# Kernel optimization log

Hardware: AMD Instinct MI355X
Metric: run time of the kernel (lower is better)

The kernel has to match this reference:

```python
import jax, jax.numpy as jnp
import numpy as np

B, S, D, H, HD = 8, 1, 4096, 32, 128
MAX_SEQ, AL, FF = 2048, 10, 11008
START_POS = 2047
EPS = 1e-5


def setup_inputs() -> dict:
    key = jax.random.key(0)
    ks = jax.random.split(key, 12)
    # real RoPE angles for the single decode position START_POS
    inv_freq = 1.0 / (10000.0 ** (np.arange(0, HD, 2, dtype=np.float32) / HD))  # [HD/2]
    ang = (np.float32(START_POS) * inv_freq)[None, :]  # [S=1, HD/2]
    return {
        "x": jax.random.normal(ks[0], (B, S, D), jnp.float32),
        "adapter": jax.random.normal(ks[1], (1, AL, D), jnp.float32),
        "cache_k": jax.random.normal(ks[2], (B, MAX_SEQ, H, HD), jnp.float32),
        "cache_v": jax.random.normal(ks[3], (B, MAX_SEQ, H, HD), jnp.float32),
        "freqs_cos": jnp.cos(jnp.asarray(ang)),
        "freqs_sin": jnp.sin(jnp.asarray(ang)),
        "wq": jax.random.normal(ks[4], (D, D), jnp.float32) * 0.02,
        "wk": jax.random.normal(ks[5], (D, D), jnp.float32) * 0.02,
        "wv": jax.random.normal(ks[6], (D, D), jnp.float32) * 0.02,
        "wo": jax.random.normal(ks[7], (D, D), jnp.float32) * 0.02,
        "gate": jax.random.normal(ks[8], (1, H, 1, 1), jnp.float32) * 0.5,
        "attn_norm_w": jnp.ones((D,), jnp.float32),
        "ffn_norm_w": jnp.ones((D,), jnp.float32),
        "w1": jax.random.normal(ks[9], (D, FF), jnp.float32) * 0.02,
        "w2": jax.random.normal(ks[10], (FF, D), jnp.float32) * 0.02,
        "w3": jax.random.normal(ks[11], (D, FF), jnp.float32) * 0.02,
        "start_pos": START_POS,
    }


def _rmsnorm(x, w, eps=EPS):
    xf = x.astype(jnp.float32)
    return (xf * jax.lax.rsqrt(jnp.mean(xf * xf, axis=-1, keepdims=True) + eps)).astype(x.dtype) * w


def _rope(t, cos, sin):
    # t: [B,S,H,HD]; pairs are interleaved as in view_as_complex(reshape(..,-1,2))
    tr = t.reshape(*t.shape[:-1], HD // 2, 2)
    a, b = tr[..., 0], tr[..., 1]
    c = cos[None, :, None, :]
    s = sin[None, :, None, :]
    out = jnp.stack([a * c - b * s, a * s + b * c], axis=-1)
    return out.reshape(t.shape)


def _sdpa(q, k, v):
    # q:[B,H,S,HD], k/v:[B,H,K,HD]
    scores = jnp.einsum("bhqd,bhkd->bhqk", q, k) / jnp.sqrt(jnp.float32(HD))
    p = jax.nn.softmax(scores.astype(jnp.float32), axis=-1).astype(q.dtype)
    return jnp.einsum("bhqk,bhkd->bhqd", p, v)


def reference(x, adapter, cache_k, cache_v, freqs_cos, freqs_sin,
              wq, wk, wv, wo, gate, attn_norm_w, ffn_norm_w, w1, w2, w3, start_pos):
    bsz, seqlen, _ = x.shape
    # --- attention sub-block ---
    xn = _rmsnorm(x, attn_norm_w)
    xq = (xn @ wq).reshape(bsz, seqlen, H, HD)
    xk = (xn @ wk).reshape(bsz, seqlen, H, HD)
    xv = (xn @ wv).reshape(bsz, seqlen, H, HD)
    xq = _rope(xq, freqs_cos, freqs_sin)
    xk = _rope(xk, freqs_cos, freqs_sin)
    # KV-cache append
    cache_k = jax.lax.dynamic_update_slice(cache_k, xk, (0, start_pos, 0, 0))
    cache_v = jax.lax.dynamic_update_slice(cache_v, xv, (0, start_pos, 0, 0))
    keys = cache_k[:, : start_pos + seqlen].transpose(0, 2, 1, 3)   # [B,H,K,HD]
    values = cache_v[:, : start_pos + seqlen].transpose(0, 2, 1, 3)
    q = xq.transpose(0, 2, 1, 3)                                     # [B,H,S,HD]
    out = _sdpa(q, keys, values)                                     # [B,H,S,HD]
    # adapter-gated cross attention (adapter keys/values: no RoPE, shared over batch)
    ak = (adapter @ wk).reshape(AL, H, HD).transpose(1, 0, 2)        # [H,AL,HD]
    av = (adapter @ wv).reshape(AL, H, HD).transpose(1, 0, 2)        # [H,AL,HD]
    a_scores = jnp.einsum("bhqd,hkd->bhqk", q, ak) / jnp.sqrt(jnp.float32(HD))
    a_p = jax.nn.softmax(a_scores.astype(jnp.float32), axis=-1).astype(q.dtype)
    a_out = jnp.einsum("bhqk,hkd->bhqd", a_p, av)
    out = out + jnp.tanh(gate) * a_out
    attn_out = out.transpose(0, 2, 1, 3).reshape(bsz, seqlen, H * HD) @ wo
    h = x + attn_out
    # --- feed-forward sub-block (SwiGLU) ---
    hn = _rmsnorm(h, ffn_norm_w)
    ffn = (jax.nn.silu(hn @ w1) * (hn @ w3)) @ w2
    return h + ffn
```

## Files before the change

kernel.cpp:

```cpp
#include <hip/hip_runtime.h>
#include <cmath>

#define D_ 4096
#define H_ 32
#define HD_ 128
#define B_ 8
#define MAXSEQ_ 2048
#define AL_ 10
#define FF_ 11008
#define SCALE_ 0.08838834764831845f
#define EPS_ 1e-5f

__global__ __launch_bounds__(256) void norm_adapter_k(const float* __restrict__ x,
                                                      const float* __restrict__ w,
                                                      const float* __restrict__ adapter,
                                                      float* __restrict__ xa) {
  int b = blockIdx.x, tid = threadIdx.x;
  if (b < 8) {
    const float* xr = x + (size_t)b * D_;
    float ss = 0.f;
    for (int i = tid; i < D_; i += 256) { float v = xr[i]; ss += v * v; }
    __shared__ float red[256];
    red[tid] = ss; __syncthreads();
    for (int s = 128; s; s >>= 1) { if (tid < s) red[tid] += red[tid + s]; __syncthreads(); }
    float r = rsqrtf(red[0] / (float)D_ + EPS_);
    float* o = xa + (size_t)b * D_;
    for (int i = tid; i < D_; i += 256) o[i] = xr[i] * r * w[i];
  } else {
    int r = b - 8;
    const float4* src = (const float4*)(adapter + (size_t)r * D_);
    float4* dst = (float4*)(xa + (size_t)(8 + r) * D_);
    for (int i = tid; i < D_ / 4; i += 256) dst[i] = src[i];
  }
}

__global__ __launch_bounds__(256) void rmsnorm_k(const float* __restrict__ in,
                                                 const float* __restrict__ w,
                                                 float* __restrict__ out) {
  int b = blockIdx.x, tid = threadIdx.x;
  const float* x = in + (size_t)b * D_;
  float ss = 0.f;
  for (int i = tid; i < D_; i += 256) { float v = x[i]; ss += v * v; }
  __shared__ float red[256];
  red[tid] = ss; __syncthreads();
  for (int s = 128; s; s >>= 1) { if (tid < s) red[tid] += red[tid + s]; __syncthreads(); }
  float r = rsqrtf(red[0] / (float)D_ + EPS_);
  float* o = out + (size_t)b * D_;
  for (int i = tid; i < D_; i += 256) o[i] = x[i] * r * w[i];
}

template<int NR, int ROWS, int CHUNK, int UNROLL>
__device__ __forceinline__ void gemv_core(
    const float4* __restrict__ W4, const float (*xs)[ROWS],
    int i0, int N4, int j4, int r0, float* __restrict__ P, size_t pb, int N) {
  float4 acc[NR];
#pragma unroll
  for (int r = 0; r < NR; ++r) acc[r] = make_float4(0.f, 0.f, 0.f, 0.f);
  for (int iu = 0; iu < CHUNK; iu += UNROLL) {
    float4 w[UNROLL];
#pragma unroll
    for (int u = 0; u < UNROLL; ++u)
      w[u] = W4[(size_t)(i0 + iu + u) * N4 + j4];
#pragma unroll
    for (int u = 0; u < UNROLL; ++u) {
#pragma unroll
      for (int r = 0; r < NR; ++r) {
        float xv = xs[iu + u][r0 + r];
        acc[r].x += xv * w[u].x; acc[r].y += xv * w[u].y;
        acc[r].z += xv * w[u].z; acc[r].w += xv * w[u].w;
      }
    }
  }
#pragma unroll
  for (int r = 0; r < NR; ++r)
    *(float4*)&P[(pb + r) * (size_t)N + (size_t)4 * j4] = acc[r];
}

template<int ROWS, int RPG, int CHUNK, int UNROLL>
__global__ __launch_bounds__(256, 1) void gemv_rs(
    const float* __restrict__ X,
    const float* __restrict__ Wa, const float* __restrict__ Wb, const float* __restrict__ Wc,
    float* __restrict__ P, int N, int K) {
  const float* W = (blockIdx.z == 0) ? Wa : (blockIdx.z == 1) ? Wb : Wc;
  __shared__ float xs[CHUNK][ROWS];
  int tid = threadIdx.x;
  int i0 = blockIdx.y * CHUNK;
  for (int idx = tid; idx < ROWS * CHUNK; idx += 256) {
    int r = idx / CHUNK, ii = idx - r * CHUNK;
    xs[ii][r] = X[(size_t)r * K + i0 + ii];
  }
  __syncthreads();
  int wave = tid >> 6, lane = tid & 63;
  int r0 = wave * RPG;
  int N4 = N >> 2;
  int j4 = blockIdx.x * 64 + lane;
  const float4* W4 = (const float4*)W;
  size_t pb = ((size_t)blockIdx.z * gridDim.y + blockIdx.y) * ROWS + r0;
  constexpr int LAST = ROWS - 3 * RPG;
  if (r0 + RPG <= ROWS)
    gemv_core<RPG, ROWS, CHUNK, UNROLL>(W4, xs, i0, N4, j4, r0, P, pb, N);
  else if (LAST > 0)
    gemv_core<(LAST > 0 ? LAST : 1), ROWS, CHUNK, UNROLL>(W4, xs, i0, N4, j4, r0, P, pb, N);
}

__global__ __launch_bounds__(256) void reduce3_rope_k(
    const float* __restrict__ P, const float* __restrict__ fc, const float* __restrict__ fs,
    float* __restrict__ Ya, float* __restrict__ Yb, float* __restrict__ Yc) {
  int z = blockIdx.z;
  int i4 = blockIdx.x * 256 + threadIdx.x;
  const float4* P4 = (const float4*)P;
  size_t base = (size_t)z * 16 * 18432 + i4;
  float4 s = make_float4(0.f, 0.f, 0.f, 0.f);
#pragma unroll
  for (int c = 0; c < 16; ++c) {
    float4 v = P4[base + (size_t)c * 18432];
    s.x += v.x; s.y += v.y; s.z += v.z; s.w += v.w;
  }
  int row = i4 >> 10;
  if (z < 2 && row < 8) {
    int c0 = (i4 & 1023) << 2;
    int p0 = (c0 & 127) >> 1;
    float ca = fc[p0], sa = fs[p0], cb = fc[p0 + 1], sb = fs[p0 + 1];
    float4 r;
    r.x = s.x * ca - s.y * sa; r.y = s.x * sa + s.y * ca;
    r.z = s.z * cb - s.w * sb; r.w = s.z * sb + s.w * cb;
    s = r;
  }
  float4* Y = (float4*)(z == 0 ? Ya : z == 1 ? Yb : Yc);
  Y[i4] = s;
}

__global__ __launch_bounds__(256) void reduceB_k(const float* __restrict__ P,
                                                 const float* __restrict__ base,
                                                 float* __restrict__ Y, int n4, int nc) {
  int i4 = blockIdx.x * 256 + threadIdx.x;
  if (i4 >= n4) return;
  const float4* P4 = (const float4*)P;
  float4 s = ((const float4*)base)[i4];
  for (int c = 0; c < nc; ++c) {
    float4 v = P4[(size_t)c * n4 + i4];
    s.x += v.x; s.y += v.y; s.z += v.z; s.w += v.w;
  }
  ((float4*)Y)[i4] = s;
}

__global__ __launch_bounds__(256) void reduce_silu_k(const float* __restrict__ P,
                                                     float* __restrict__ gb) {
  int i4 = blockIdx.x * 256 + threadIdx.x;
  const float4* P4 = (const float4*)P;
  float4 a = make_float4(0.f, 0.f, 0.f, 0.f);
  float4 b = make_float4(0.f, 0.f, 0.f, 0.f);
#pragma unroll
  for (int c = 0; c < 8; ++c) {
    float4 u = P4[(size_t)c * 22016 + i4];
    float4 v = P4[(size_t)(8 + c) * 22016 + i4];
    a.x += u.x; a.y += u.y; a.z += u.z; a.w += u.w;
    b.x += v.x; b.y += v.y; b.z += v.z; b.w += v.w;
  }
  float4 o;
  o.x = (a.x / (1.f + __expf(-a.x))) * b.x;
  o.y = (a.y / (1.f + __expf(-a.y))) * b.y;
  o.z = (a.z / (1.f + __expf(-a.z))) * b.z;
  o.w = (a.w / (1.f + __expf(-a.w))) * b.w;
  ((float4*)gb)[i4] = o;
}

__global__ __launch_bounds__(256) void attn_partial(
    const float* __restrict__ qp,
    const float* __restrict__ ck,
    const float* __restrict__ cv,
    float* __restrict__ part) {
  int idx = blockIdx.x;
  int c = idx & 7, bh = idx >> 3;
  int h = bh & 31, b = bh >> 5;
  int tid = threadIdx.x, wave = tid >> 6, lane = tid & 63;
  int half = lane >> 5, l32 = lane & 31;
  int t0 = c * 256 + wave * 64;
  const float4 qv = *(const float4*)&qp[(size_t)b * D_ + h * HD_ + 4 * l32];
  const size_t kvbase = ((size_t)b * MAXSEQ_) * (H_ * HD_) + (size_t)h * HD_ + 4 * l32;
  float m = -INFINITY, l = 0.f;
  float4 o = make_float4(0.f, 0.f, 0.f, 0.f);
#pragma unroll 4
  for (int i = 0; i < 32; ++i) {
    int t = t0 + 2 * i + half;
    size_t off = kvbase + (size_t)t * (H_ * HD_);
    float4 kv = *(const float4*)&ck[off];
    float s = qv.x * kv.x + qv.y * kv.y + qv.z * kv.z + qv.w * kv.w;
    s += __shfl_xor(s, 16); s += __shfl_xor(s, 8);
    s += __shfl_xor(s, 4);  s += __shfl_xor(s, 2); s += __shfl_xor(s, 1);
    s *= SCALE_;
    if (t == MAXSEQ_ - 1) s = -1e30f;
    float mn = fmaxf(m, s);
    float r = __expf(m - mn), p = __expf(s - mn);
    float4 vv = *(const float4*)&cv[off];
    o.x = o.x * r + p * vv.x; o.y = o.y * r + p * vv.y;
    o.z = o.z * r + p * vv.z; o.w = o.w * r + p * vv.w;
    l = l * r + p; m = mn;
  }
  float mo = __shfl_xor(m, 32);
  float M = fmaxf(m, mo);
  float e = __expf(m - M);
  o.x *= e; o.y *= e; o.z *= e; o.w *= e; l *= e;
  o.x += __shfl_xor(o.x, 32); o.y += __shfl_xor(o.y, 32);
  o.z += __shfl_xor(o.z, 32); o.w += __shfl_xor(o.w, 32);
  l += __shfl_xor(l, 32);
  float* po = &part[((size_t)idx * 4 + wave) * 132];
  if (lane == 0) { po[0] = M; po[1] = l; }
  if (half == 0) *(float4*)&po[4 + 4 * l32] = o;
}

__global__ __launch_bounds__(128) void attn_combine(
    const float* __restrict__ part,
    const float* __restrict__ qp,
    const float* __restrict__ kvk,
    const float* __restrict__ kvv,
    const float* __restrict__ gate,
    float* __restrict__ attn) {
  int bh = blockIdx.x;
  int h = bh & 31, b = bh >> 5;
  int tid = threadIdx.x;
  const float* pb = &part[(size_t)bh * 32 * 132];
  __shared__ float sm[32], sl[32];
  if (tid < 32) { sm[tid] = pb[tid * 132]; sl[tid] = pb[tid * 132 + 1]; }
  __syncthreads();
  float M = -INFINITY;
  for (int c = 0; c < 32; ++c) M = fmaxf(M, sm[c]);
  float L = 0.f, O = 0.f;
  for (int c = 0; c < 32; ++c) {
    float e = __expf(sm[c] - M);
    L += e * sl[c];
    O += e * pb[c * 132 + 4 + tid];
  }
  size_t qi = (size_t)b * D_ + h * HD_ + tid;
  float qd = qp[qi];
  __shared__ float red[128];
  __shared__ float sa[10];
  red[tid] = qd * kvk[qi]; __syncthreads();
  for (int s = 64; s; s >>= 1) { if (tid < s) red[tid] += red[tid + s]; __syncthreads(); }
  float s_new = red[0] * SCALE_;
  __syncthreads();
  float M2 = fmaxf(M, s_new);
  float eM = __expf(M - M2), eN = __expf(s_new - M2);
  L = L * eM + eN;
  O = O * eM + eN * kvv[qi];
  float main_out = O / L;
  for (int j = 0; j < 10; ++j) {
    float prod = qd * kvk[(size_t)(8 + j) * D_ + h * HD_ + tid];
    red[tid] = prod; __syncthreads();
    for (int s = 64; s; s >>= 1) { if (tid < s) red[tid] += red[tid + s]; __syncthreads(); }
    if (tid == 0) sa[j] = red[0] * SCALE_;
    __syncthreads();
  }
  float ma = -INFINITY;
  for (int j = 0; j < 10; ++j) ma = fmaxf(ma, sa[j]);
  float la = 0.f, pj[10];
  for (int j = 0; j < 10; ++j) { pj[j] = __expf(sa[j] - ma); la += pj[j]; }
  float ao = 0.f;
  for (int j = 0; j < 10; ++j) ao += pj[j] * kvv[(size_t)(8 + j) * D_ + h * HD_ + tid];
  ao /= la;
  float g = tanhf(gate[h]);
  attn[qi] = main_out + g * ao;
}

extern "C" void kernel_launch(void* const* d_in, const int* in_sizes, int n_in,
                              void* d_out, int out_size, void* d_ws, size_t ws_size,
                              hipStream_t stream) {
  (void)in_sizes; (void)n_in; (void)out_size; (void)ws_size;
  const float* x       = (const float*)d_in[0];
  const float* adapter = (const float*)d_in[1];
  const float* ck      = (const float*)d_in[2];
  const float* cv      = (const float*)d_in[3];
  const float* fc      = (const float*)d_in[4];
  const float* fs      = (const float*)d_in[5];
  const float* wq      = (const float*)d_in[6];
  const float* wk      = (const float*)d_in[7];
  const float* wv      = (const float*)d_in[8];
  const float* wo      = (const float*)d_in[9];
  const float* gate    = (const float*)d_in[10];
  const float* anw     = (const float*)d_in[11];
  const float* fnw     = (const float*)d_in[12];
  const float* w1      = (const float*)d_in[13];
  const float* w2      = (const float*)d_in[14];
  const float* w3      = (const float*)d_in[15];
  float* out = (float*)d_out;

  float* ws      = (float*)d_ws;
  float* xa      = ws;
  float* qp      = xa + 18 * D_;
  float* kp      = qp + 18 * D_;
  float* vp      = kp + 18 * D_;
  float* attn    = vp + 18 * D_;
  float* hbuf    = attn + 8 * D_;
  float* hn      = hbuf + 8 * D_;
  float* gb      = hn + 8 * D_;
  float* scratch = gb + 8 * FF_;

  norm_adapter_k<<<18, 256, 0, stream>>>(x, anw, adapter, xa);
  gemv_rs<18, 5, 256, 16><<<dim3(16, 16, 3), 256, 0, stream>>>(xa, wq, wk, wv, scratch, D_, D_);
  reduce3_rope_k<<<dim3(72, 1, 3), 256, 0, stream>>>(scratch, fc, fs, qp, kp, vp);
  attn_partial<<<2048, 256, 0, stream>>>(qp, ck, cv, scratch);
  attn_combine<<<256, 128, 0, stream>>>(scratch, qp, kp, vp, gate, attn);
  gemv_rs<8, 2, 128, 16><<<dim3(16, 32, 1), 256, 0, stream>>>(attn, wo, wo, wo, scratch, D_, D_);
  reduceB_k<<<32, 256, 0, stream>>>(scratch, x, hbuf, 8192, 32);
  rmsnorm_k<<<8, 256, 0, stream>>>(hbuf, fnw, hn);
  gemv_rs<8, 2, 512, 16><<<dim3(43, 8, 2), 256, 0, stream>>>(hn, w1, w3, w3, scratch, FF_, D_);
  reduce_silu_k<<<86, 256, 0, stream>>>(scratch, gb);
  gemv_rs<8, 2, 344, 8><<<dim3(16, 32, 1), 256, 0, stream>>>(gb, w2, w2, w2, scratch, D_, FF_);
  reduceB_k<<<32, 256, 0, stream>>>(scratch, hbuf, out, 8192, 32);
}
```

Before: 398.3 us.

## Restructure decode attention so each block streams full KV rows across all heads

Measured after the change: 412.6 us. 1.04x slower.

```diff
diff --git a/kernel.cpp b/kernel.cpp
--- a/kernel.cpp
+++ b/kernel.cpp
@@ -8,6 +8,7 @@
 #define MAXSEQ_ 2048
 #define AL_ 10
 #define FF_ 11008
+#define NC_ 128
 #define SCALE_ 0.08838834764831845f
 #define EPS_ 1e-5f
 
@@ -130,10 +131,10 @@
   Y[i4] = s;
 }
 
-__global__ __launch_bounds__(256) void reduceB_k(const float* __restrict__ P,
+__global__ __launch_bounds__(128) void reduceB_k(const float* __restrict__ P,
                                                  const float* __restrict__ base,
                                                  float* __restrict__ Y, int n4, int nc) {
-  int i4 = blockIdx.x * 256 + threadIdx.x;
+  int i4 = blockIdx.x * 128 + threadIdx.x;
   if (i4 >= n4) return;
   const float4* P4 = (const float4*)P;
   float4 s = ((const float4*)base)[i4];
@@ -144,9 +145,9 @@
   ((float4*)Y)[i4] = s;
 }
 
-__global__ __launch_bounds__(256) void reduce_silu_k(const float* __restrict__ P,
+__global__ __launch_bounds__(128) void reduce_silu_k(const float* __restrict__ P,
                                                      float* __restrict__ gb) {
-  int i4 = blockIdx.x * 256 + threadIdx.x;
+  int i4 = blockIdx.x * 128 + threadIdx.x;
   const float4* P4 = (const float4*)P;
   float4 a = make_float4(0.f, 0.f, 0.f, 0.f);
   float4 b = make_float4(0.f, 0.f, 0.f, 0.f);
@@ -165,48 +166,48 @@
   ((float4*)gb)[i4] = o;
 }
 
-__global__ __launch_bounds__(256) void attn_partial(
+__global__ __launch_bounds__(256, 4) void attn_partial(
     const float* __restrict__ qp,
     const float* __restrict__ ck,
     const float* __restrict__ cv,
     float* __restrict__ part) {
-  int idx = blockIdx.x;
-  int c = idx & 7, bh = idx >> 3;
-  int h = bh & 31, b = bh >> 5;
+  int c = blockIdx.x, b = blockIdx.y;
   int tid = threadIdx.x, wave = tid >> 6, lane = tid & 63;
-  int half = lane >> 5, l32 = lane & 31;
-  int t0 = c * 256 + wave * 64;
-  const float4 qv = *(const float4*)&qp[(size_t)b * D_ + h * HD_ + 4 * l32];
-  const size_t kvbase = ((size_t)b * MAXSEQ_) * (H_ * HD_) + (size_t)h * HD_ + 4 * l32;
+  int hl = lane >> 3;
+  int h = wave * 8 + hl;
+  int d0 = (lane & 7) << 4;
+  const float4* q4 = (const float4*)&qp[(size_t)b * D_ + h * HD_ + d0];
+  float4 q0 = q4[0], q1 = q4[1], q2 = q4[2], q3 = q4[3];
+  int t0 = c * 16;
+  size_t base = ((size_t)(b * MAXSEQ_ + t0)) * D_ + (size_t)h * HD_ + d0;
   float m = -INFINITY, l = 0.f;
-  float4 o = make_float4(0.f, 0.f, 0.f, 0.f);
+  float4 o0 = make_float4(0.f,0.f,0.f,0.f), o1 = o0, o2 = o0, o3 = o0;
 #pragma unroll 4
-  for (int i = 0; i < 32; ++i) {
-    int t = t0 + 2 * i + half;
-    size_t off = kvbase + (size_t)t * (H_ * HD_);
-    float4 kv = *(const float4*)&ck[off];
-    float s = qv.x * kv.x + qv.y * kv.y + qv.z * kv.z + qv.w * kv.w;
-    s += __shfl_xor(s, 16); s += __shfl_xor(s, 8);
-    s += __shfl_xor(s, 4);  s += __shfl_xor(s, 2); s += __shfl_xor(s, 1);
+  for (int i = 0; i < 16; ++i) {
+    size_t off = base + (size_t)i * D_;
+    const float4* kp4 = (const float4*)&ck[off];
+    float4 k0 = kp4[0], k1 = kp4[1], k2 = kp4[2], k3 = kp4[3];
+    float s = q0.x*k0.x + q0.y*k0.y + q0.z*k0.z + q0.w*k0.w
+            + q1.x*k1.x + q1.y*k1.y + q1.z*k1.z + q1.w*k1.w
+            + q2.x*k2.x + q2.y*k2.y + q2.z*k2.z + q2.w*k2.w
+            + q3.x*k3.x + q3.y*k3.y + q3.z*k3.z + q3.w*k3.w;
+    s += __shfl_xor(s, 1); s += __shfl_xor(s, 2); s += __shfl_xor(s, 4);
     s *= SCALE_;
-    if (t == MAXSEQ_ - 1) s = -1e30f;
+    if (t0 + i == MAXSEQ_ - 1) s = -1e30f;
     float mn = fmaxf(m, s);
     float r = __expf(m - mn), p = __expf(s - mn);
-    float4 vv = *(const float4*)&cv[off];
-    o.x = o.x * r + p * vv.x; o.y = o.y * r + p * vv.y;
-    o.z = o.z * r + p * vv.z; o.w = o.w * r + p * vv.w;
+    const float4* vp4 = (const float4*)&cv[off];
+    float4 v0 = vp4[0], v1 = vp4[1], v2 = vp4[2], v3 = vp4[3];
+    o0.x = o0.x*r + p*v0.x; o0.y = o0.y*r + p*v0.y; o0.z = o0.z*r + p*v0.z; o0.w = o0.w*r + p*v0.w;
+    o1.x = o1.x*r + p*v1.x; o1.y = o1.y*r + p*v1.y; o1.z = o1.z*r + p*v1.z; o1.w = o1.w*r + p*v1.w;
+    o2.x = o2.x*r + p*v2.x; o2.y = o2.y*r + p*v2.y; o2.z = o2.z*r + p*v2.z; o2.w = o2.w*r + p*v2.w;
+    o3.x = o3.x*r + p*v3.x; o3.y = o3.y*r + p*v3.y; o3.z = o3.z*r + p*v3.z; o3.w = o3.w*r + p*v3.w;
     l = l * r + p; m = mn;
   }
-  float mo = __shfl_xor(m, 32);
-  float M = fmaxf(m, mo);
-  float e = __expf(m - M);
-  o.x *= e; o.y *= e; o.z *= e; o.w *= e; l *= e;
-  o.x += __shfl_xor(o.x, 32); o.y += __shfl_xor(o.y, 32);
-  o.z += __shfl_xor(o.z, 32); o.w += __shfl_xor(o.w, 32);
-  l += __shfl_xor(l, 32);
-  float* po = &part[((size_t)idx * 4 + wave) * 132];
-  if (lane == 0) { po[0] = M; po[1] = l; }
-  if (half == 0) *(float4*)&po[4 + 4 * l32] = o;
+  float* po = &part[(((size_t)b * NC_ + c) * H_ + h) * 132];
+  if ((lane & 7) == 0) { po[0] = m; po[1] = l; }
+  float4* po4 = (float4*)&po[4 + d0];
+  po4[0] = o0; po4[1] = o1; po4[2] = o2; po4[3] = o3;
 }
 
 __global__ __launch_bounds__(128) void attn_combine(
@@ -219,40 +220,47 @@
   int bh = blockIdx.x;
   int h = bh & 31, b = bh >> 5;
   int tid = threadIdx.x;
-  const float* pb = &part[(size_t)bh * 32 * 132];
-  __shared__ float sm[32], sl[32];
-  if (tid < 32) { sm[tid] = pb[tid * 132]; sl[tid] = pb[tid * 132 + 1]; }
+  int wave = tid >> 6, lane = tid & 63;
+  const size_t cs = (size_t)H_ * 132;
+  const float* pb = &part[((size_t)b * NC_ * H_ + h) * 132];
+  __shared__ float sm[NC_], sl[NC_], red[NC_];
+  sm[tid] = pb[cs * tid];
+  sl[tid] = pb[cs * tid + 1];
   __syncthreads();
-  float M = -INFINITY;
-  for (int c = 0; c < 32; ++c) M = fmaxf(M, sm[c]);
+  red[tid] = sm[tid]; __syncthreads();
+  for (int s = 64; s; s >>= 1) { if (tid < s) red[tid] = fmaxf(red[tid], red[tid + s]); __syncthreads(); }
+  float M = red[0];
   float L = 0.f, O = 0.f;
-  for (int c = 0; c < 32; ++c) {
-    float e = __expf(sm[c] - M);
-    L += e * sl[c];
-    O += e * pb[c * 132 + 4 + tid];
+#pragma unroll 4
+  for (int c2 = 0; c2 < NC_; ++c2) {
+    float e = __expf(sm[c2] - M);
+    L += e * sl[c2];
+    O += e * pb[cs * c2 + 4 + tid];
   }
   size_t qi = (size_t)b * D_ + h * HD_ + tid;
   float qd = qp[qi];
-  __shared__ float red[128];
-  __shared__ float sa[10];
-  red[tid] = qd * kvk[qi]; __syncthreads();
-  for (int s = 64; s; s >>= 1) { if (tid < s) red[tid] += red[tid + s]; __syncthreads(); }
-  float s_new = red[0] * SCALE_;
+  __shared__ float s2[2][12];
+  {
+    float pr = qd * kvk[qi];
+    pr += __shfl_xor(pr, 32); pr += __shfl_xor(pr, 16); pr += __shfl_xor(pr, 8);
+    pr += __shfl_xor(pr, 4);  pr += __shfl_xor(pr, 2);  pr += __shfl_xor(pr, 1);
+    if (lane == 0) s2[wave][10] = pr;
+  }
+  for (int j = 0; j < 10; ++j) {
+    float pr = qd * kvk[(size_t)(8 + j) * D_ + h * HD_ + tid];
+    pr += __shfl_xor(pr, 32); pr += __shfl_xor(pr, 16); pr += __shfl_xor(pr, 8);
+    pr += __shfl_xor(pr, 4);  pr += __shfl_xor(pr, 2);  pr += __shfl_xor(pr, 1);
+    if (lane == 0) s2[wave][j] = pr;
+  }
   __syncthreads();
+  float s_new = (s2[0][10] + s2[1][10]) * SCALE_;
   float M2 = fmaxf(M, s_new);
   float eM = __expf(M - M2), eN = __expf(s_new - M2);
   L = L * eM + eN;
   O = O * eM + eN * kvv[qi];
   float main_out = O / L;
-  for (int j = 0; j < 10; ++j) {
-    float prod = qd * kvk[(size_t)(8 + j) * D_ + h * HD_ + tid];
-    red[tid] = prod; __syncthreads();
-    for (int s = 64; s; s >>= 1) { if (tid < s) red[tid] += red[tid + s]; __syncthreads(); }
-    if (tid == 0) sa[j] = red[0] * SCALE_;
-    __syncthreads();
-  }
-  float ma = -INFINITY;
-  for (int j = 0; j < 10; ++j) ma = fmaxf(ma, sa[j]);
+  float ma = -INFINITY, sa[10];
+  for (int j = 0; j < 10; ++j) { sa[j] = (s2[0][j] + s2[1][j]) * SCALE_; ma = fmaxf(ma, sa[j]); }
   float la = 0.f, pj[10];
   for (int j = 0; j < 10; ++j) { pj[j] = __expf(sa[j] - ma); la += pj[j]; }
   float ao = 0.f;
@@ -298,13 +306,13 @@
   norm_adapter_k<<<18, 256, 0, stream>>>(x, anw, adapter, xa);
   gemv_rs<18, 5, 256, 16><<<dim3(16, 16, 3), 256, 0, stream>>>(xa, wq, wk, wv, scratch, D_, D_);
   reduce3_rope_k<<<dim3(72, 1, 3), 256, 0, stream>>>(scratch, fc, fs, qp, kp, vp);
-  attn_partial<<<2048, 256, 0, stream>>>(qp, ck, cv, scratch);
+  attn_partial<<<dim3(NC_, 8), 256, 0, stream>>>(qp, ck, cv, scratch);
   attn_combine<<<256, 128, 0, stream>>>(scratch, qp, kp, vp, gate, attn);
   gemv_rs<8, 2, 128, 16><<<dim3(16, 32, 1), 256, 0, stream>>>(attn, wo, wo, wo, scratch, D_, D_);
-  reduceB_k<<<32, 256, 0, stream>>>(scratch, x, hbuf, 8192, 32);
+  reduceB_k<<<64, 128, 0, stream>>>(scratch, x, hbuf, 8192, 32);
   rmsnorm_k<<<8, 256, 0, stream>>>(hbuf, fnw, hn);
   gemv_rs<8, 2, 512, 16><<<dim3(43, 8, 2), 256, 0, stream>>>(hn, w1, w3, w3, scratch, FF_, D_);
-  reduce_silu_k<<<86, 256, 0, stream>>>(scratch, gb);
+  reduce_silu_k<<<172, 128, 0, stream>>>(scratch, gb);
   gemv_rs<8, 2, 344, 8><<<dim3(16, 32, 1), 256, 0, stream>>>(gb, w2, w2, w2, scratch, D_, FF_);
-  reduceB_k<<<32, 256, 0, stream>>>(scratch, hbuf, out, 8192, 32);
-}
+  reduceB_k<<<64, 128, 0, stream>>>(scratch, hbuf, out, 8192, 32);
+}
```

## Fuse decoder layer into one persistent cooperative kernel with grid syncs

Applied to the files above, without the earlier changes.

Result: slower. 777.7 us (+95.3%).

```diff
diff --git a/kernel.cpp b/kernel.cpp
--- a/kernel.cpp
+++ b/kernel.cpp
@@ -1,5 +1,8 @@
 #include <hip/hip_runtime.h>
+#include <hip/hip_cooperative_groups.h>
 #include <cmath>
+
+namespace cg = cooperative_groups;
 
 #define D_ 4096
 #define H_ 32
@@ -8,8 +11,305 @@
 #define MAXSEQ_ 2048
 #define AL_ 10
 #define FF_ 11008
+#define NBLK 256
 #define SCALE_ 0.08838834764831845f
 #define EPS_ 1e-5f
+
+template<int NR, int ROWS, int CHUNK, int UNROLL>
+__device__ __forceinline__ void gemv_core(
+    const float4* __restrict__ W4, const float (*xs)[ROWS],
+    int i0, int N4, int j4, int r0, float* __restrict__ P, size_t pb, int N) {
+  float4 acc[NR];
+#pragma unroll
+  for (int r = 0; r < NR; ++r) acc[r] = make_float4(0.f, 0.f, 0.f, 0.f);
+  for (int iu = 0; iu < CHUNK; iu += UNROLL) {
+    float4 w[UNROLL];
+#pragma unroll
+    for (int u = 0; u < UNROLL; ++u)
+      w[u] = W4[(size_t)(i0 + iu + u) * N4 + j4];
+#pragma unroll
+    for (int u = 0; u < UNROLL; ++u) {
+#pragma unroll
+      for (int r = 0; r < NR; ++r) {
+        float xv = xs[iu + u][r0 + r];
+        acc[r].x += xv * w[u].x; acc[r].y += xv * w[u].y;
+        acc[r].z += xv * w[u].z; acc[r].w += xv * w[u].w;
+      }
+    }
+  }
+#pragma unroll
+  for (int r = 0; r < NR; ++r)
+    *(float4*)&P[(pb + r) * (size_t)N + (size_t)4 * j4] = acc[r];
+}
+
+template<int ROWS, int RPG, int CHUNK, int UNROLL>
+__device__ __forceinline__ void gemv_phase(
+    const float* __restrict__ X, const float* __restrict__ W, float* __restrict__ P,
+    int N, int K, int bx, int by, int zoff, float* smem, int tid) {
+  int i0 = by * CHUNK;
+  for (int idx = tid; idx < ROWS * CHUNK; idx += 256) {
+    int r = idx / CHUNK, ii = idx - r * CHUNK;
+    smem[ii * ROWS + r] = X[(size_t)r * K + i0 + ii];
+  }
+  __syncthreads();
+  int wave = tid >> 6, lane = tid & 63;
+  int r0 = wave * RPG;
+  int N4 = N >> 2;
+  int j4 = bx * 64 + lane;
+  size_t pb = (size_t)zoff * ROWS + r0;
+  const float (*xs)[ROWS] = (const float (*)[ROWS])smem;
+  constexpr int LAST = ROWS - 3 * RPG;
+  if (r0 + RPG <= ROWS)
+    gemv_core<RPG, ROWS, CHUNK, UNROLL>((const float4*)W, xs, i0, N4, j4, r0, P, pb, N);
+  else if (LAST > 0)
+    gemv_core<(LAST > 0 ? LAST : 1), ROWS, CHUNK, UNROLL>((const float4*)W, xs, i0, N4, j4, r0, P, pb, N);
+  __syncthreads();
+}
+
+__device__ __forceinline__ void rmsnorm_phase(const float* __restrict__ in,
+                                              const float* __restrict__ w,
+                                              float* __restrict__ outp,
+                                              int b, float* red, int tid) {
+  const float* xr = in + (size_t)b * D_;
+  float ss = 0.f;
+  for (int i = tid; i < D_; i += 256) { float v = xr[i]; ss += v * v; }
+  red[tid] = ss; __syncthreads();
+  for (int s = 128; s; s >>= 1) { if (tid < s) red[tid] += red[tid + s]; __syncthreads(); }
+  float r = rsqrtf(red[0] / (float)D_ + EPS_);
+  __syncthreads();
+  float* o = outp + (size_t)b * D_;
+  for (int i = tid; i < D_; i += 256) o[i] = xr[i] * r * w[i];
+}
+
+__global__ __launch_bounds__(256, 1) void mega_k(
+    const float* __restrict__ x, const float* __restrict__ adapter,
+    const float* __restrict__ ck, const float* __restrict__ cv,
+    const float* __restrict__ fc, const float* __restrict__ fs,
+    const float* __restrict__ wq, const float* __restrict__ wk,
+    const float* __restrict__ wv, const float* __restrict__ wo,
+    const float* __restrict__ gate, const float* __restrict__ anw,
+    const float* __restrict__ fnw, const float* __restrict__ w1,
+    const float* __restrict__ w2, const float* __restrict__ w3,
+    float* __restrict__ out, float* __restrict__ ws) {
+  cg::grid_group grid = cg::this_grid();
+  __shared__ float smem[4608];
+  int blk = blockIdx.x, tid = threadIdx.x;
+
+  float* xa      = ws;
+  float* qp      = xa + 18 * D_;
+  float* kp      = qp + 18 * D_;
+  float* vp      = kp + 18 * D_;
+  float* attn    = vp + 18 * D_;
+  float* hbuf    = attn + 8 * D_;
+  float* hn      = hbuf + 8 * D_;
+  float* gb      = hn + 8 * D_;
+  float* scratch = gb + 8 * FF_;
+
+  if (blk < 8) {
+    rmsnorm_phase(x, anw, xa, blk, smem, tid);
+  } else if (blk < 18) {
+    int r = blk - 8;
+    const float4* src = (const float4*)(adapter + (size_t)r * D_);
+    float4* dst = (float4*)(xa + (size_t)(8 + r) * D_);
+    for (int i = tid; i < D_ / 4; i += 256) dst[i] = src[i];
+  }
+  grid.sync();
+
+  for (int vb = blk; vb < 768; vb += NBLK) {
+    int bx = vb & 15, by = (vb >> 4) & 15, z = vb >> 8;
+    const float* W = (z == 0) ? wq : (z == 1) ? wk : wv;
+    gemv_phase<18, 5, 256, 16>(xa, W, scratch, D_, D_, bx, by, z * 16 + by, smem, tid);
+  }
+  grid.sync();
+
+  for (int vb = blk; vb < 216; vb += NBLK) {
+    int z = vb / 72, xb = vb - z * 72;
+    int i4 = xb * 256 + tid;
+    const float4* P4 = (const float4*)scratch;
+    size_t base = (size_t)z * 16 * 18432 + i4;
+    float4 s = make_float4(0.f, 0.f, 0.f, 0.f);
+#pragma unroll
+    for (int c = 0; c < 16; ++c) {
+      float4 v = P4[base + (size_t)c * 18432];
+      s.x += v.x; s.y += v.y; s.z += v.z; s.w += v.w;
+    }
+    int row = i4 >> 10;
+    if (z < 2 && row < 8) {
+      int c0 = (i4 & 1023) << 2;
+      int p0 = (c0 & 127) >> 1;
+      float ca = fc[p0], sa = fs[p0], cb = fc[p0 + 1], sb = fs[p0 + 1];
+      float4 r;
+      r.x = s.x * ca - s.y * sa; r.y = s.x * sa + s.y * ca;
+      r.z = s.z * cb - s.w * sb; r.w = s.z * sb + s.w * cb;
+      s = r;
+    }
+    float4* Y = (float4*)(z == 0 ? qp : z == 1 ? kp : vp);
+    Y[i4] = s;
+  }
+  grid.sync();
+
+  {
+    int b = blk >> 5, c = blk & 31;
+    int wave = tid >> 6, lane = tid & 63;
+    int hl = lane >> 3, h = wave * 8 + hl;
+    int d0 = (lane & 7) << 4;
+    const float4* q4 = (const float4*)&qp[(size_t)b * D_ + h * HD_ + d0];
+    float4 q0 = q4[0], q1 = q4[1], q2 = q4[2], q3 = q4[3];
+    int t0 = c * 64;
+    size_t base = ((size_t)(b * MAXSEQ_ + t0)) * D_ + (size_t)h * HD_ + d0;
+    float m = -INFINITY, l = 0.f;
+    float4 o0 = make_float4(0.f,0.f,0.f,0.f), o1 = o0, o2 = o0, o3 = o0;
+#pragma unroll 4
+    for (int i = 0; i < 64; ++i) {
+      size_t off = base + (size_t)i * D_;
+      const float4* kp4 = (const float4*)&ck[off];
+      float4 k0 = kp4[0], k1 = kp4[1], k2 = kp4[2], k3 = kp4[3];
+      float s = q0.x*k0.x + q0.y*k0.y + q0.z*k0.z + q0.w*k0.w
+              + q1.x*k1.x + q1.y*k1.y + q1.z*k1.z + q1.w*k1.w
+              + q2.x*k2.x + q2.y*k2.y + q2.z*k2.z + q2.w*k2.w
+              + q3.x*k3.x + q3.y*k3.y + q3.z*k3.z + q3.w*k3.w;
+      s += __shfl_xor(s, 1); s += __shfl_xor(s, 2); s += __shfl_xor(s, 4);
+      s *= SCALE_;
+      if (t0 + i == MAXSEQ_ - 1) s = -1e30f;
+      float mn = fmaxf(m, s);
+      float r = __expf(m - mn), p = __expf(s - mn);
+      const float4* vp4 = (const float4*)&cv[off];
+      float4 v0 = vp4[0], v1 = vp4[1], v2 = vp4[2], v3 = vp4[3];
+      o0.x = o0.x*r + p*v0.x; o0.y = o0.y*r + p*v0.y; o0.z = o0.z*r + p*v0.z; o0.w = o0.w*r + p*v0.w;
+      o1.x = o1.x*r + p*v1.x; o1.y = o1.y*r + p*v1.y; o1.z = o1.z*r + p*v1.z; o1.w = o1.w*r + p*v1.w;
+      o2.x = o2.x*r + p*v2.x; o2.y = o2.y*r + p*v2.y; o2.z = o2.z*r + p*v2.z; o2.w = o2.w*r + p*v2.w;
+      o3.x = o3.x*r + p*v3.x; o3.y = o3.y*r + p*v3.y; o3.z = o3.z*r + p*v3.z; o3.w = o3.w*r + p*v3.w;
+      l = l * r + p; m = mn;
+    }
+    float* po = &scratch[(((size_t)b * 32 + c) * H_ + h) * 132];
+    if ((lane & 7) == 0) { po[0] = m; po[1] = l; }
+    float4* po4 = (float4*)&po[4 + d0];
+    po4[0] = o0; po4[1] = o1; po4[2] = o2; po4[3] = o3;
+  }
+  grid.sync();
+
+  for (int vb = blk; vb < 128; vb += NBLK) {
+    int half = tid >> 7, t2 = tid & 127;
+    int bh = vb * 2 + half;
+    int h = bh & 31, b = bh >> 5;
+    int wave2 = t2 >> 6, lane = tid & 63;
+    const size_t cs = (size_t)H_ * 132;
+    const float* pb = &scratch[((size_t)b * 32 * H_ + h) * 132];
+    float* sm = smem + half * 128;
+    float* sl = sm + 32;
+    float* s2 = sl + 32;
+    if (t2 < 32) { sm[t2] = pb[cs * t2]; sl[t2] = pb[cs * t2 + 1]; }
+    __syncthreads();
+    float M = -INFINITY;
+    for (int c2 = 0; c2 < 32; ++c2) M = fmaxf(M, sm[c2]);
+    float L = 0.f, O = 0.f;
+#pragma unroll 4
+    for (int c2 = 0; c2 < 32; ++c2) {
+      float e = __expf(sm[c2] - M);
+      L += e * sl[c2];
+      O += e * pb[cs * c2 + 4 + t2];
+    }
+    size_t qi = (size_t)b * D_ + h * HD_ + t2;
+    float qd = qp[qi];
+    {
+      float pr = qd * kp[qi];
+      pr += __shfl_xor(pr, 32); pr += __shfl_xor(pr, 16); pr += __shfl_xor(pr, 8);
+      pr += __shfl_xor(pr, 4);  pr += __shfl_xor(pr, 2);  pr += __shfl_xor(pr, 1);
+      if (lane == 0) s2[wave2 * 12 + 10] = pr;
+    }
+    for (int j = 0; j < 10; ++j) {
+      float pr = qd * kp[(size_t)(8 + j) * D_ + h * HD_ + t2];
+      pr += __shfl_xor(pr, 32); pr += __shfl_xor(pr, 16); pr += __shfl_xor(pr, 8);
+      pr += __shfl_xor(pr, 4);  pr += __shfl_xor(pr, 2);  pr += __shfl_xor(pr, 1);
+      if (lane == 0) s2[wave2 * 12 + j] = pr;
+    }
+    __syncthreads();
+    float s_new = (s2[10] + s2[12 + 10]) * SCALE_;
+    float M2 = fmaxf(M, s_new);
+    float eM = __expf(M - M2), eN = __expf(s_new - M2);
+    L = L * eM + eN;
+    O = O * eM + eN * vp[qi];
+    float main_out = O / L;
+    float ma = -INFINITY, sa[10];
+    for (int j = 0; j < 10; ++j) { sa[j] = (s2[j] + s2[12 + j]) * SCALE_; ma = fmaxf(ma, sa[j]); }
+    float la = 0.f, pj[10];
+    for (int j = 0; j < 10; ++j) { pj[j] = __expf(sa[j] - ma); la += pj[j]; }
+    float ao = 0.f;
+    for (int j = 0; j < 10; ++j) ao += pj[j] * vp[(size_t)(8 + j) * D_ + h * HD_ + t2];
+    ao /= la;
+    float g = tanhf(gate[h]);
+    attn[qi] = main_out + g * ao;
+    __syncthreads();
+  }
+  grid.sync();
+
+  for (int vb = blk; vb < 512; vb += NBLK) {
+    int bx = vb & 15, by = vb >> 4;
+    gemv_phase<8, 2, 128, 16>(attn, wo, scratch, D_, D_, bx, by, by, smem, tid);
+  }
+  grid.sync();
+
+  for (int vb = blk; vb < 32; vb += NBLK) {
+    int i4 = vb * 256 + tid;
+    const float4* P4 = (const float4*)scratch;
+    float4 s = ((const float4*)x)[i4];
+    for (int c = 0; c < 32; ++c) {
+      float4 v = P4[(size_t)c * 8192 + i4];
+      s.x += v.x; s.y += v.y; s.z += v.z; s.w += v.w;
+    }
+    ((float4*)hbuf)[i4] = s;
+  }
+  grid.sync();
+
+  if (blk < 8) rmsnorm_phase(hbuf, fnw, hn, blk, smem, tid);
+  grid.sync();
+
+  for (int vb = blk; vb < 688; vb += NBLK) {
+    int bx = vb % 43, r = vb / 43;
+    int by = r & 7, z = r >> 3;
+    const float* W = z ? w3 : w1;
+    gemv_phase<8, 2, 512, 16>(hn, W, scratch, FF_, D_, bx, by, z * 8 + by, smem, tid);
+  }
+  grid.sync();
+
+  for (int vb = blk; vb < 86; vb += NBLK) {
+    int i4 = vb * 256 + tid;
+    const float4* P4 = (const float4*)scratch;
+    float4 a = make_float4(0.f, 0.f, 0.f, 0.f);
+    float4 b = make_float4(0.f, 0.f, 0.f, 0.f);
+#pragma unroll
+    for (int c = 0; c < 8; ++c) {
+      float4 u = P4[(size_t)c * 22016 + i4];
+      float4 v = P4[(size_t)(8 + c) * 22016 + i4];
+      a.x += u.x; a.y += u.y; a.z += u.z; a.w += u.w;
+      b.x += v.x; b.y += v.y; b.z += v.z; b.w += v.w;
+    }
+    float4 o;
+    o.x = (a.x / (1.f + __expf(-a.x))) * b.x;
+    o.y = (a.y / (1.f + __expf(-a.y))) * b.y;
+    o.z = (a.z / (1.f + __expf(-a.z))) * b.z;
+    o.w = (a.w / (1.f + __expf(-a.w))) * b.w;
+    ((float4*)gb)[i4] = o;
+  }
+  grid.sync();
+
+  for (int vb = blk; vb < 512; vb += NBLK) {
+    int bx = vb & 15, by = vb >> 4;
+    gemv_phase<8, 2, 344, 8>(gb, w2, scratch, D_, FF_, bx, by, by, smem, tid);
+  }
+  grid.sync();
+
+  for (int vb = blk; vb < 32; vb += NBLK) {
+    int i4 = vb * 256 + tid;
+    const float4* P4 = (const float4*)scratch;
+    float4 s = ((const float4*)hbuf)[i4];
+    for (int c = 0; c < 32; ++c) {
+      float4 v = P4[(size_t)c * 8192 + i4];
+      s.x += v.x; s.y += v.y; s.z += v.z; s.w += v.w;
+    }
+    ((float4*)out)[i4] = s;
+  }
+}
 
 __global__ __launch_bounds__(256) void norm_adapter_k(const float* __restrict__ x,
                                                       const float* __restrict__ w,
@@ -49,33 +349,6 @@
   for (int i = tid; i < D_; i += 256) o[i] = x[i] * r * w[i];
 }
 
-template<int NR, int ROWS, int CHUNK, int UNROLL>
-__device__ __forceinline__ void gemv_core(
-    const float4* __restrict__ W4, const float (*xs)[ROWS],
-    int i0, int N4, int j4, int r0, float* __restrict__ P, size_t pb, int N) {
-  float4 acc[NR];
-#pragma unroll
-  for (int r = 0; r < NR; ++r) acc[r] = make_float4(0.f, 0.f, 0.f, 0.f);
-  for (int iu = 0; iu < CHUNK; iu += UNROLL) {
-    float4 w[UNROLL];
-#pragma unroll
-    for (int u = 0; u < UNROLL; ++u)
-      w[u] = W4[(size_t)(i0 + iu + u) * N4 + j4];
-#pragma unroll
-    for (int u = 0; u < UNROLL; ++u) {
-#pragma unroll
-      for (int r = 0; r < NR; ++r) {
-        float xv = xs[iu + u][r0 + r];
-        acc[r].x += xv * w[u].x; acc[r].y += xv * w[u].y;
-        acc[r].z += xv * w[u].z; acc[r].w += xv * w[u].w;
-      }
-    }
-  }
-#pragma unroll
-  for (int r = 0; r < NR; ++r)
-    *(float4*)&P[(pb + r) * (size_t)N + (size_t)4 * j4] = acc[r];
-}
-
 template<int ROWS, int RPG, int CHUNK, int UNROLL>
 __global__ __launch_bounds__(256, 1) void gemv_rs(
     const float* __restrict__ X,
@@ -165,11 +438,9 @@
   ((float4*)gb)[i4] = o;
 }
 
-__global__ __launch_bounds__(256) void attn_partial(
-    const float* __restrict__ qp,
-    const float* __restrict__ ck,
-    const float* __restrict__ cv,
-    float* __restrict__ part) {
+__global__ __launch_bounds__(256) void attn_partial_fb(
+    const float* __restrict__ qp, const float* __restrict__ ck,
+    const float* __restrict__ cv, float* __restrict__ part) {
   int idx = blockIdx.x;
   int c = idx & 7, bh = idx >> 3;
   int h = bh & 31, b = bh >> 5;
@@ -209,13 +480,10 @@
   if (half == 0) *(float4*)&po[4 + 4 * l32] = o;
 }
 
-__global__ __launch_bounds__(128) void attn_combine(
-    const float* __restrict__ part,
-    const float* __restrict__ qp,
-    const float* __restrict__ kvk,
-    const float* __restrict__ kvv,
-    const float* __restrict__ gate,
-    float* __restrict__ attn) {
+__global__ __launch_bounds__(128) void attn_combine_fb(
+    const float* __restrict__ part, const float* __restrict__ qp,
+    const float* __restrict__ kvk, const float* __restrict__ kvv,
+    const float* __restrict__ gate, float* __restrict__ attn) {
   int bh = blockIdx.x;
   int h = bh & 31, b = bh >> 5;
   int tid = threadIdx.x;
@@ -283,28 +551,36 @@
   const float* w2      = (const float*)d_in[14];
   const float* w3      = (const float*)d_in[15];
   float* out = (float*)d_out;
-
-  float* ws      = (float*)d_ws;
-  float* xa      = ws;
-  float* qp      = xa + 18 * D_;
-  float* kp      = qp + 18 * D_;
-  float* vp      = kp + 18 * D_;
-  float* attn    = vp + 18 * D_;
-  float* hbuf    = attn + 8 * D_;
-  float* hn      = hbuf + 8 * D_;
-  float* gb      = hn + 8 * D_;
-  float* scratch = gb + 8 * FF_;
-
-  norm_adapter_k<<<18, 256, 0, stream>>>(x, anw, adapter, xa);
-  gemv_rs<18, 5, 256, 16><<<dim3(16, 16, 3), 256, 0, stream>>>(xa, wq, wk, wv, scratch, D_, D_);
-  reduce3_rope_k<<<dim3(72, 1, 3), 256, 0, stream>>>(scratch, fc, fs, qp, kp, vp);
-  attn_partial<<<2048, 256, 0, stream>>>(qp, ck, cv, scratch);
-  attn_combine<<<256, 128, 0, stream>>>(scratch, qp, kp, vp, gate, attn);
-  gemv_rs<8, 2, 128, 16><<<dim3(16, 32, 1), 256, 0, stream>>>(attn, wo, wo, wo, scratch, D_, D_);
-  reduceB_k<<<32, 256, 0, stream>>>(scratch, x, hbuf, 8192, 32);
-  rmsnorm_k<<<8, 256, 0, stream>>>(hbuf, fnw, hn);
-  gemv_rs<8, 2, 512, 16><<<dim3(43, 8, 2), 256, 0, stream>>>(hn, w1, w3, w3, scratch, FF_, D_);
-  reduce_silu_k<<<86, 256, 0, stream>>>(scratch, gb);
-  gemv_rs<8, 2, 344, 8><<<dim3(16, 32, 1), 256, 0, stream>>>(gb, w2, w2, w2, scratch, D_, FF_);
-  reduceB_k<<<32, 256, 0, stream>>>(scratch, hbuf, out, 8192, 32);
-}
+  float* ws  = (float*)d_ws;
+
+  void* args[] = {
+    (void*)&x, (void*)&adapter, (void*)&ck, (void*)&cv, (void*)&fc, (void*)&fs,
+    (void*)&wq, (void*)&wk, (void*)&wv, (void*)&wo, (void*)&gate, (void*)&anw,
+    (void*)&fnw, (void*)&w1, (void*)&w2, (void*)&w3, (void*)&out, (void*)&ws
+  };
+  hipError_t err = hipLaunchCooperativeKernel((void*)mega_k, dim3(NBLK), dim3(256), args, 0, stream);
+  if (err != hipSuccess) {
+    float* xa      = ws;
+    float* qp      = xa + 18 * D_;
+    float* kp      = qp + 18 * D_;
+    float* vp      = kp + 18 * D_;
+    float* attn    = vp + 18 * D_;
+    float* hbuf    = attn + 8 * D_;
+    float* hn      = hbuf + 8 * D_;
+    float* gb      = hn + 8 * D_;
+    float* scratch = gb + 8 * FF_;
+
+    norm_adapter_k<<<18, 256, 0, stream>>>(x, anw, adapter, xa);
+    gemv_rs<18, 5, 256, 16><<<dim3(16, 16, 3), 256, 0, stream>>>(xa, wq, wk, wv, scratch, D_, D_);
+    reduce3_rope_k<<<dim3(72, 1, 3), 256, 0, stream>>>(scratch, fc, fs, qp, kp, vp);
+    attn_partial_fb<<<2048, 256, 0, stream>>>(qp, ck, cv, scratch);
+    attn_combine_fb<<<256, 128, 0, stream>>>(scratch, qp, kp, vp, gate, attn);
+    gemv_rs<8, 2, 128, 16><<<dim3(16, 32, 1), 256, 0, stream>>>(attn, wo, wo, wo, scratch, D_, D_);
+    reduceB_k<<<32, 256, 0, stream>>>(scratch, x, hbuf, 8192, 32);
+    rmsnorm_k<<<8, 256, 0, stream>>>(hbuf, fnw, hn);
+    gemv_rs<8, 2, 512, 16><<<dim3(43, 8, 2), 256, 0, stream>>>(hn, w1, w3, w3, scratch, FF_, D_);
+    reduce_silu_k<<<86, 256, 0, stream>>>(scratch, gb);
+    gemv_rs<8, 2, 344, 8><<<dim3(16, 32, 1), 256, 0, stream>>>(gb, w2, w2, w2, scratch, D_, FF_);
+    reduceB_k<<<32, 256, 0, stream>>>(scratch, hbuf, out, 8192, 32);
+  }
+}
```

## Widen split-K across GEMVs when workspace allows and fuse residual reduce with RMSNorm

Applied to the files above, without the earlier changes.

Result: slower. 452.5 us (+13.6%).

```diff
diff --git a/kernel.cpp b/kernel.cpp
--- a/kernel.cpp
+++ b/kernel.cpp
@@ -10,6 +10,7 @@
 #define FF_ 11008
 #define SCALE_ 0.08838834764831845f
 #define EPS_ 1e-5f
+#define PSTRIDE 160
 
 __global__ __launch_bounds__(256) void norm_adapter_k(const float* __restrict__ x,
                                                       const float* __restrict__ w,
@@ -34,21 +35,6 @@
   }
 }
 
-__global__ __launch_bounds__(256) void rmsnorm_k(const float* __restrict__ in,
-                                                 const float* __restrict__ w,
-                                                 float* __restrict__ out) {
-  int b = blockIdx.x, tid = threadIdx.x;
-  const float* x = in + (size_t)b * D_;
-  float ss = 0.f;
-  for (int i = tid; i < D_; i += 256) { float v = x[i]; ss += v * v; }
-  __shared__ float red[256];
-  red[tid] = ss; __syncthreads();
-  for (int s = 128; s; s >>= 1) { if (tid < s) red[tid] += red[tid + s]; __syncthreads(); }
-  float r = rsqrtf(red[0] / (float)D_ + EPS_);
-  float* o = out + (size_t)b * D_;
-  for (int i = tid; i < D_; i += 256) o[i] = x[i] * r * w[i];
-}
-
 template<int NR, int ROWS, int CHUNK, int UNROLL>
 __device__ __forceinline__ void gemv_core(
     const float4* __restrict__ W4, const float (*xs)[ROWS],
@@ -105,14 +91,13 @@
 
 __global__ __launch_bounds__(256) void reduce3_rope_k(
     const float* __restrict__ P, const float* __restrict__ fc, const float* __restrict__ fs,
-    float* __restrict__ Ya, float* __restrict__ Yb, float* __restrict__ Yc) {
+    float* __restrict__ Ya, float* __restrict__ Yb, float* __restrict__ Yc, int nc) {
   int z = blockIdx.z;
   int i4 = blockIdx.x * 256 + threadIdx.x;
   const float4* P4 = (const float4*)P;
-  size_t base = (size_t)z * 16 * 18432 + i4;
+  size_t base = (size_t)z * nc * 18432 + i4;
   float4 s = make_float4(0.f, 0.f, 0.f, 0.f);
-#pragma unroll
-  for (int c = 0; c < 16; ++c) {
+  for (int c = 0; c < nc; ++c) {
     float4 v = P4[base + (size_t)c * 18432];
     s.x += v.x; s.y += v.y; s.z += v.z; s.w += v.w;
   }
@@ -144,16 +129,39 @@
   ((float4*)Y)[i4] = s;
 }
 
+__global__ __launch_bounds__(1024) void h_norm_k(const float* __restrict__ P,
+                                                 const float* __restrict__ x,
+                                                 const float* __restrict__ w,
+                                                 float* __restrict__ hbuf,
+                                                 float* __restrict__ hn, int nc) {
+  int b = blockIdx.x, tid = threadIdx.x;
+  const float4* P4 = (const float4*)P;
+  float4 s = ((const float4*)x)[b * 1024 + tid];
+  for (int c = 0; c < nc; ++c) {
+    float4 v = P4[((size_t)c * 8 + b) * 1024 + tid];
+    s.x += v.x; s.y += v.y; s.z += v.z; s.w += v.w;
+  }
+  ((float4*)hbuf)[b * 1024 + tid] = s;
+  float ss = s.x * s.x + s.y * s.y + s.z * s.z + s.w * s.w;
+  __shared__ float red[1024];
+  red[tid] = ss; __syncthreads();
+  for (int st = 512; st; st >>= 1) { if (tid < st) red[tid] += red[tid + st]; __syncthreads(); }
+  float r = rsqrtf(red[0] / (float)D_ + EPS_);
+  float4 wv = ((const float4*)w)[tid];
+  float4 o;
+  o.x = s.x * r * wv.x; o.y = s.y * r * wv.y; o.z = s.z * r * wv.z; o.w = s.w * r * wv.w;
+  ((float4*)hn)[b * 1024 + tid] = o;
+}
+
 __global__ __launch_bounds__(256) void reduce_silu_k(const float* __restrict__ P,
-                                                     float* __restrict__ gb) {
+                                                     float* __restrict__ gb, int nc) {
   int i4 = blockIdx.x * 256 + threadIdx.x;
   const float4* P4 = (const float4*)P;
   float4 a = make_float4(0.f, 0.f, 0.f, 0.f);
   float4 b = make_float4(0.f, 0.f, 0.f, 0.f);
-#pragma unroll
-  for (int c = 0; c < 8; ++c) {
+  for (int c = 0; c < nc; ++c) {
     float4 u = P4[(size_t)c * 22016 + i4];
-    float4 v = P4[(size_t)(8 + c) * 22016 + i4];
+    float4 v = P4[(size_t)(nc + c) * 22016 + i4];
     a.x += u.x; a.y += u.y; a.z += u.z; a.w += u.w;
     b.x += v.x; b.y += v.y; b.z += v.z; b.w += v.w;
   }
@@ -204,9 +212,9 @@
   o.x += __shfl_xor(o.x, 32); o.y += __shfl_xor(o.y, 32);
   o.z += __shfl_xor(o.z, 32); o.w += __shfl_xor(o.w, 32);
   l += __shfl_xor(l, 32);
-  float* po = &part[((size_t)idx * 4 + wave) * 132];
+  float* po = &part[((size_t)idx * 4 + wave) * PSTRIDE];
   if (lane == 0) { po[0] = M; po[1] = l; }
-  if (half == 0) *(float4*)&po[4 + 4 * l32] = o;
+  if (half == 0) *(float4*)&po[32 + 4 * l32] = o;
 }
 
 __global__ __launch_bounds__(128) void attn_combine(
@@ -219,9 +227,9 @@
   int bh = blockIdx.x;
   int h = bh & 31, b = bh >> 5;
   int tid = threadIdx.x;
-  const float* pb = &part[(size_t)bh * 32 * 132];
+  const float* pb = &part[(size_t)bh * 32 * PSTRIDE];
   __shared__ float sm[32], sl[32];
-  if (tid < 32) { sm[tid] = pb[tid * 132]; sl[tid] = pb[tid * 132 + 1]; }
+  if (tid < 32) { sm[tid] = pb[tid * PSTRIDE]; sl[tid] = pb[tid * PSTRIDE + 1]; }
   __syncthreads();
   float M = -INFINITY;
   for (int c = 0; c < 32; ++c) M = fmaxf(M, sm[c]);
@@ -229,7 +237,7 @@
   for (int c = 0; c < 32; ++c) {
     float e = __expf(sm[c] - M);
     L += e * sl[c];
-    O += e * pb[c * 132 + 4 + tid];
+    O += e * pb[c * PSTRIDE + 32 + tid];
   }
   size_t qi = (size_t)b * D_ + h * HD_ + tid;
   float qd = qp[qi];
@@ -265,7 +273,7 @@
 extern "C" void kernel_launch(void* const* d_in, const int* in_sizes, int n_in,
                               void* d_out, int out_size, void* d_ws, size_t ws_size,
                               hipStream_t stream) {
-  (void)in_sizes; (void)n_in; (void)out_size; (void)ws_size;
+  (void)in_sizes; (void)n_in; (void)out_size;
   const float* x       = (const float*)d_in[0];
   const float* adapter = (const float*)d_in[1];
   const float* ck      = (const float*)d_in[2];
@@ -294,17 +302,38 @@
   float* hn      = hbuf + 8 * D_;
   float* gb      = hn + 8 * D_;
   float* scratch = gb + 8 * FF_;
+  bool wide = ws_size >= (size_t)40 * 1024 * 1024;
 
   norm_adapter_k<<<18, 256, 0, stream>>>(x, anw, adapter, xa);
-  gemv_rs<18, 5, 256, 16><<<dim3(16, 16, 3), 256, 0, stream>>>(xa, wq, wk, wv, scratch, D_, D_);
-  reduce3_rope_k<<<dim3(72, 1, 3), 256, 0, stream>>>(scratch, fc, fs, qp, kp, vp);
+
+  if (wide) {
+    gemv_rs<18, 5, 128, 8><<<dim3(16, 32, 3), 256, 0, stream>>>(xa, wq, wk, wv, scratch, D_, D_);
+    reduce3_rope_k<<<dim3(72, 1, 3), 256, 0, stream>>>(scratch, fc, fs, qp, kp, vp, 32);
+  } else {
+    gemv_rs<18, 5, 256, 16><<<dim3(16, 16, 3), 256, 0, stream>>>(xa, wq, wk, wv, scratch, D_, D_);
+    reduce3_rope_k<<<dim3(72, 1, 3), 256, 0, stream>>>(scratch, fc, fs, qp, kp, vp, 16);
+  }
   attn_partial<<<2048, 256, 0, stream>>>(qp, ck, cv, scratch);
   attn_combine<<<256, 128, 0, stream>>>(scratch, qp, kp, vp, gate, attn);
-  gemv_rs<8, 2, 128, 16><<<dim3(16, 32, 1), 256, 0, stream>>>(attn, wo, wo, wo, scratch, D_, D_);
-  reduceB_k<<<32, 256, 0, stream>>>(scratch, x, hbuf, 8192, 32);
-  rmsnorm_k<<<8, 256, 0, stream>>>(hbuf, fnw, hn);
-  gemv_rs<8, 2, 512, 16><<<dim3(43, 8, 2), 256, 0, stream>>>(hn, w1, w3, w3, scratch, FF_, D_);
-  reduce_silu_k<<<86, 256, 0, stream>>>(scratch, gb);
-  gemv_rs<8, 2, 344, 8><<<dim3(16, 32, 1), 256, 0, stream>>>(gb, w2, w2, w2, scratch, D_, FF_);
-  reduceB_k<<<32, 256, 0, stream>>>(scratch, hbuf, out, 8192, 32);
-}
+  if (wide) {
+    gemv_rs<8, 2, 64, 8><<<dim3(16, 64, 1), 256, 0, stream>>>(attn, wo, wo, wo, scratch, D_, D_);
+    h_norm_k<<<8, 1024, 0, stream>>>(scratch, x, fnw, hbuf, hn, 64);
+  } else {
+    gemv_rs<8, 2, 128, 16><<<dim3(16, 32, 1), 256, 0, stream>>>(attn, wo, wo, wo, scratch, D_, D_);
+    h_norm_k<<<8, 1024, 0, stream>>>(scratch, x, fnw, hbuf, hn, 32);
+  }
+  if (wide) {
+    gemv_rs<8, 2, 128, 8><<<dim3(43, 32, 2), 256, 0, stream>>>(hn, w1, w3, w3, scratch, FF_, D_);
+    reduce_silu_k<<<86, 256, 0, stream>>>(scratch, gb, 32);
+  } else {
+    gemv_rs<8, 2, 512, 16><<<dim3(43, 8, 2), 256, 0, stream>>>(hn, w1, w3, w3, scratch, FF_, D_);
+    reduce_silu_k<<<86, 256, 0, stream>>>(scratch, gb, 8);
+  }
+  if (wide) {
+    gemv_rs<8, 2, 128, 8><<<dim3(16, 86, 1), 256, 0, stream>>>(gb, w2, w2, w2, scratch, D_, FF_);
+    reduceB_k<<<32, 256, 0, stream>>>(scratch, hbuf, out, 8192, 86);
+  } else {
+    gemv_rs<8, 2, 344, 8><<<dim3(16, 32, 1), 256, 0, stream>>>(gb, w2, w2, w2, scratch, D_, FF_);
+    reduceB_k<<<32, 256, 0, stream>>>(scratch, hbuf, out, 8192, 32);
+  }
+}
```
